# Optimization experiments

Measured on AMD Instinct MI355X. Metric: run time of the kernel, lower is better.

Reference implementation:

```python
import jax, jax.numpy as jnp
import numpy as np

TOPK = 2


def _conv2d(x, w, b):
    # x: (B, Cin, H, W), w: (Cout, Cin, 3, 3), SAME padding (padding=1)
    y = jax.lax.conv_general_dilated(
        x, w, window_strides=(1, 1), padding='SAME',
        dimension_numbers=('NCHW', 'OIHW', 'NCHW'))
    return y + b[None, :, None, None]


def _msunit(x2d, c1w, c1b, c2w, c2b):
    # TimesNet-style 2D unit: conv(1->d_model) -> GELU -> conv(d_model->1)
    h = jax.nn.gelu(_conv2d(x2d, c1w, c1b))
    return _conv2d(h, c2w, c2b)


def setup_inputs():
    B, T, H, DM = 256, 2048, 720, 64
    key = jax.random.key(0)
    ks = jax.random.split(key, 5)
    x = jax.random.normal(ks[0], (B, 1, T), jnp.float32)
    conv1_w = jax.random.normal(ks[1], (DM, 1, 3, 3), jnp.float32) * 0.1
    conv1_b = jnp.zeros((DM,), jnp.float32)
    conv2_w = jax.random.normal(ks[2], (1, DM, 3, 3), jnp.float32) * 0.1
    conv2_b = jnp.zeros((1,), jnp.float32)
    head_w = jax.random.normal(ks[3], (H, T), jnp.float32) * 0.02
    head_b = jnp.zeros((H,), jnp.float32)
    return {'x': x, 'conv1_w': conv1_w, 'conv1_b': conv1_b,
            'conv2_w': conv2_w, 'conv2_b': conv2_b,
            'head_w': head_w, 'head_b': head_b}


def reference(x, conv1_w, conv1_b, conv2_w, conv2_b, head_w, head_b):
    B, _, T = x.shape
    # FFT amplitude spectrum, batch-averaged, drop DC bin
    amp = jnp.abs(jnp.fft.rfft(x[:, 0, :], axis=-1)).mean(0)[1:]
    vals, idx = jax.lax.top_k(amp, TOPK)
    # data-dependent period selection (mirrors .item() calls in torch -> Python ints)
    freqs = np.asarray(idx) + 1
    P_list = [max(1, int(round(T / int(f)))) for f in freqs]
    weights = jax.nn.softmax(vals.astype(x.dtype))
    y = jnp.zeros_like(x)
    for i, P in enumerate(P_list):
        cols = (T + P - 1) // P
        pad = P * cols - T
        xp = jnp.pad(x, ((0, 0), (0, 0), (0, pad)))
        x2d = xp.reshape(B, 1, cols, P).transpose(0, 1, 3, 2)  # (B,1,P,cols)
        y2d = _msunit(x2d, conv1_w, conv1_b, conv2_w, conv2_b)  # (B,1,P,cols)
        y1d = y2d.transpose(0, 1, 3, 2).reshape(B, 1, cols * P)[..., :T]
        y = y + weights[i] * y1d
    out = y[:, 0, :] @ head_w.T + head_b  # (B, horizon)
    return out
```

## Files before the change

### kernel.cpp

```cpp
#include <hip/hip_runtime.h>
#include <math.h>

#define T_LEN   2048
#define NB      256
#define N_FREQ  1024
#define DMODEL  64
#define HORIZON 720

#define WS_AMP  64
#define WS_Y0   2048
#define WS_Y1   (2048 + NB * T_LEN)

#define PMAX_FAST 191
#define CHUNK   1024
#define NCHUNK  2
#define HSTRIDE 1412
#define ZSLOT   1408
#define XSMAX   1824
#define ZXS     (XSMAX - 1)

typedef _Float16 h4 __attribute__((ext_vector_type(4)));
typedef float    fx4 __attribute__((ext_vector_type(4)));

__device__ __forceinline__ float gelu_fast(float a) {
    float a2 = a * a;
    float z  = a * fmaf(-0.07135481627159498f, a2, -1.5957691216057308f);
    float e  = __expf(z);
    return a * __builtin_amdgcn_rcpf(1.0f + e);
}

__device__ __forceinline__ float2 cmul(float2 a, float2 b) {
    return make_float2(a.x * b.x - a.y * b.y, a.x * b.y + a.y * b.x);
}

__device__ __forceinline__ unsigned magic_div(unsigned d) {
    return (unsigned)((0x100000000ULL + d - 1) / d);
}

__device__ __forceinline__ void compute_meta(const float* __restrict__ amp,
                                             float* sf, int* si, int tid,
                                             int& P1, int& cols1, int& P2, int& cols2,
                                             float& wg1, float& wg2) {
    float* v1s = sf;        float* v2s = sf + 256;
    int*   i1s = si;        int*   i2s = si + 256;
    float4 v4 = ((const float4*)amp)[tid];
    float vv[4] = {v4.x, v4.y, v4.z, v4.w};
    float v1 = -1e30f, v2 = -1e30f; int i1 = 1 << 30, i2 = 1 << 30;
    #pragma unroll
    for (int u = 0; u < 4; ++u) {
        int j = tid * 4 + u;
        float v = vv[u];
        if (v > v1) { v2 = v1; i2 = i1; v1 = v; i1 = j; }
        else if (v > v2) { v2 = v; i2 = j; }
    }
    v1s[tid] = v1; i1s[tid] = i1; v2s[tid] = v2; i2s[tid] = i2;
    __syncthreads();
    for (int st = 128; st > 0; st >>= 1) {
        if (tid < st) {
            float w1 = v1s[tid + st]; int j1 = i1s[tid + st];
            float w2 = v2s[tid + st]; int j2 = i2s[tid + st];
            float a1 = v1s[tid];      int a1i = i1s[tid];
            float a2 = v2s[tid];      int a2i = i2s[tid];
            float n1, n2; int n1i, n2i;
            bool w1_first = (w1 > a1) || (w1 == a1 && j1 < a1i);
            if (w1_first) {
                n1 = w1; n1i = j1;
                bool a1_next = (a1 > w2) || (a1 == w2 && a1i < j2);
                if (a1_next) { n2 = a1; n2i = a1i; } else { n2 = w2; n2i = j2; }
            } else {
                n1 = a1; n1i = a1i;
                bool w1_next = (w1 > a2) || (w1 == a2 && j1 < a2i);
                if (w1_next) { n2 = w1; n2i = j1; } else { n2 = a2; n2i = a2i; }
            }
            v1s[tid] = n1; i1s[tid] = n1i; v2s[tid] = n2; i2s[tid] = n2i;
        }
        __syncthreads();
    }
    float v1f = v1s[0], v2f = v2s[0];
    int f1 = i1s[0] + 1, f2 = i2s[0] + 1;
    __syncthreads();
    P1 = (int)llround(2048.0 / (double)f1); if (P1 < 1) P1 = 1;
    P2 = (int)llround(2048.0 / (double)f2); if (P2 < 1) P2 = 1;
    cols1 = (T_LEN + P1 - 1) / P1;
    cols2 = (T_LEN + P2 - 1) / P2;
    float mx = fmaxf(v1f, v2f);
    float e1 = __expf(v1f - mx), e2 = __expf(v2f - mx);
    float inv = 1.0f / (e1 + e2);
    wg1 = e1 * inv; wg2 = e2 * inv;
}

__global__ __launch_bounds__(256) void fft_amp_kernel(const float* __restrict__ x,
                                                      float* __restrict__ amp,
                                                      float* __restrict__ out) {
    __shared__ float2 buf0[1024];
    __shared__ float2 buf1[1024];
    __shared__ float2 tw[512];
    const int tid = threadIdx.x;
    const int b = blockIdx.x;

    if (tid < 180) {
        const int zi = b * 180 + tid;
        ((float4*)out)[zi] = make_float4(0.f, 0.f, 0.f, 0.f);
    }

    {
        float s, c;
        __sincosf((float)tid * 6.135923151542565e-3f, &s, &c);
        tw[tid] = make_float2(c, -s);
        __sincosf((float)(tid + 256) * 6.135923151542565e-3f, &s, &c);
        tw[tid + 256] = make_float2(c, -s);
    }
    const float2* xz = (const float2*)(x + b * T_LEN);
    buf0[tid]       = xz[tid];
    buf0[tid + 256] = xz[tid + 256];
    buf0[tid + 512] = xz[tid + 512];
    buf0[tid + 768] = xz[tid + 768];
    __syncthreads();

    float2* src = buf0;
    float2* dst = buf1;
    for (int s = 0; s < 10; s += 2) {
        const int Ns = 1 << s;
        const int j1 = tid;
        const int q  = j1 & (Ns - 1);
        const int hi = j1 >> s;
        float2 A = src[j1];
        float2 B = src[j1 + 512];
        float2 C = src[j1 + 256];
        float2 D = src[j1 + 768];
        float2 w  = tw[q << (9 - s)];
        float2 wB = cmul(w, B);
        float2 wD = cmul(w, D);
        float2 P0 = make_float2(A.x + wB.x, A.y + wB.y);
        float2 P1 = make_float2(A.x - wB.x, A.y - wB.y);
        float2 Q0 = make_float2(C.x + wD.x, C.y + wD.y);
        float2 Q1 = make_float2(C.x - wD.x, C.y - wD.y);
        float2 wa = tw[q << (8 - s)];
        float2 wb = tw[(q + Ns) << (8 - s)];
        float2 t0 = cmul(wa, Q0);
        float2 t1 = cmul(wb, Q1);
        const int O = (hi << (s + 2)) + q;
        dst[O]          = make_float2(P0.x + t0.x, P0.y + t0.y);
        dst[O + 2 * Ns] = make_float2(P0.x - t0.x, P0.y - t0.y);
        dst[O + Ns]     = make_float2(P1.x + t1.x, P1.y + t1.y);
        dst[O + 3 * Ns] = make_float2(P1.x - t1.x, P1.y - t1.y);
        __syncthreads();
        float2* tmp = src; src = dst; dst = tmp;
    }
    const int rot = (b * 8) & 1023;
    #pragma unroll
    for (int j = 0; j < 4; ++j) {
        const int kk = (tid + j * 256 + rot) & 1023;
        const int k  = kk + 1;
        float mag;
        if (k == 1024) {
            float2 Z0 = src[0];
            mag = fabsf(Z0.x - Z0.y) * (1.0f / 256.0f);
        } else {
            float2 Zk = src[k];
            float2 Zn = src[1024 - k];
            float Ax = 0.5f * (Zk.x + Zn.x), Ay = 0.5f * (Zk.y - Zn.y);
            float Bx = 0.5f * (Zk.y + Zn.y), By = -0.5f * (Zk.x - Zn.x);
            float sn, cs;
            __sincosf((float)k * 3.0679615757712823e-3f, &sn, &cs);
            float Xx = Ax + cs * Bx + sn * By;
            float Xy = Ay + cs * By - sn * Bx;
            mag = sqrtf(Xx * Xx + Xy * Xy) * (1.0f / 256.0f);
        }
        atomicAdd(amp + kk, mag);
    }
}

__global__ __launch_bounds__(256) void conv_fast_kernel(
    const float* __restrict__ x,
    const float* __restrict__ w1, const float* __restrict__ b1,
    const float* __restrict__ w2, const float* __restrict__ b2,
    const float* __restrict__ amp,
    float* __restrict__ ws)
{
    __shared__ float xs[XSMAX];
    __shared__ _Float16 dk[9][HSTRIDE];

    const int tid = threadIdx.x;

    int P1, cols1, P2, cols2; float wg1, wg2;
    compute_meta(amp, xs, (int*)(xs + 512), tid, P1, cols1, P2, cols2, wg1, wg2);

    if (blockIdx.x == 0 && blockIdx.y == 0 && tid == 0) {
        int* mi = (int*)ws;
        mi[0] = P1; mi[1] = cols1; mi[2] = P2; mi[3] = cols2;
        ws[4] = wg1; ws[5] = wg2;
    }

    const int per  = blockIdx.y;
    const int P    = per == 0 ? P1 : P2;
    const int cols = per == 0 ? cols1 : cols2;
    if (P > PMAX_FAST || P < 2) return;
    const float wgt = per == 0 ? wg1 : wg2;
    float* yout = ws + (per == 0 ? WS_Y0 : WS_Y1);

    const int b   = blockIdx.x >> 1;
    const int ci  = blockIdx.x & 1;
    const int t0  = ci * CHUNK;
    const int U0  = t0 - (P + 1);
    const int HN  = CHUNK + 2 * P + 2;
    const int X0  = t0 - (2 * P + 2);
    const int XN  = CHUNK + 4 * P + 4;
    const unsigned MP = magic_div((unsigned)P);

    __syncthreads();
    const int bT = b * T_LEN;
    for (int j = tid; j < XSMAX; j += 256) {
        int t = X0 + j;
        xs[j] = (j < XN && t >= 0 && t < T_LEN) ? x[bT + t] : 0.f;
    }
    __syncthreads();

    const int lane = tid & 63;
    const int wv   = tid >> 6;
    const int lm   = lane & 15;
    const int lg   = lane >> 4;

    h4  w1f[4], w2f[4];
    fx4 b1f[4];
    #pragma unroll
    for (int t = 0; t < 4; ++t) {
        #pragma unroll
        for (int i = 0; i < 4; ++i) {
            const int k = lg * 4 + i;
            w1f[t][i] = (_Float16)((k < 9) ? w1[(t * 16 + lm) * 9 + k] : 0.f);
            w2f[t][i] = (_Float16)((lm < 9) ? w2[(t * 16 + k) * 9 + lm] : 0.f);
            b1f[t][i] = b1[t * 16 + k];
        }
    }

    const int HN16 = (HN + 15) >> 4;
    const fx4 zf4 = {0.f, 0.f, 0.f, 0.f};

    for (int nt = wv; nt < HN16; nt += 4) {
        const int ih = nt * 16 + lm;
        const int u  = U0 + ih;
        const int uu = u < 0 ? 0 : u;
        const int cc = (int)__umulhi((unsigned)uu, MP);
        const int pp = uu - cc * P;
        const bool rm = pp > 0, rp = pp < P - 1, cm = cc > 0, cp = (cc + 1) < cols;
        const int ibase = ih + P + 1;
        h4 xb;
        #pragma unroll
        for (int j = 0; j < 4; ++j) {
            const int tap = lg * 4 + j;
            const int q = (tap * 86) >> 8;
            const int r = tap - q * 3;
            const bool ok = (tap < 9)
                && (q > 0 || rm) && (q < 2 || rp)
                && (r > 0 || cm) && (r < 2 || cp);
            const int addr = ok ? (ibase + (r - 1) * P + (q - 1)) : ZXS;
            xb[j] = (_Float16)xs[addr];
        }
        fx4 h0 = __builtin_amdgcn_mfma_f32_16x16x16f16(w1f[0], xb, b1f[0], 0, 0, 0);
        fx4 h1 = __builtin_amdgcn_mfma_f32_16x16x16f16(w1f[1], xb, b1f[1], 0, 0, 0);
        fx4 h2 = __builtin_amdgcn_mfma_f32_16x16x16f16(w1f[2], xb, b1f[2], 0, 0, 0);
        fx4 h3 = __builtin_amdgcn_mfma_f32_16x16x16f16(w1f[3], xb, b1f[3], 0, 0, 0);
        h4 g0, g1, g2, g3;
        #pragma unroll
        for (int i = 0; i < 4; ++i) {
            g0[i] = (_Float16)gelu_fast(h0[i]);
            g1[i] = (_Float16)gelu_fast(h1[i]);
            g2[i] = (_Float16)gelu_fast(h2[i]);
            g3[i] = (_Float16)gelu_fast(h3[i]);
        }
        fx4 da = __builtin_amdgcn_mfma_f32_16x16x16f16(w2f[0], g0, zf4, 0, 0, 0);
        fx4 db = __builtin_amdgcn_mfma_f32_16x16x16f16(w2f[1], g1, zf4, 0, 0, 0);
        da = __builtin_amdgcn_mfma_f32_16x16x16f16(w2f[2], g2, da, 0, 0, 0);
        db = __builtin_amdgcn_mfma_f32_16x16x16f16(w2f[3], g3, db, 0, 0, 0);
        if (ih < HN) {
            #pragma unroll
            for (int i = 0; i < 4; ++i) {
                const int row = lg * 4 + i;
                if (row < 9) dk[row][ih] = (_Float16)(da[i] + db[i]);
            }
        }
    }
    if (tid < 9) dk[tid][ZSLOT] = (_Float16)0.f;
    __syncthreads();

    const float bias2 = b2[0];
    #pragma unroll
    for (int o = 0; o < 4; ++o) {
        const int t = t0 + tid + o * 256;
        const int iout = tid + o * 256 + (P + 1);
        const int cc = (int)__umulhi((unsigned)t, MP);
        const int pp = t - cc * P;
        const bool rm = pp > 0, rp = pp < P - 1, cm = cc > 0, cp = (cc + 1) < cols;
        const int i0 = (rm && cm) ? iout - P - 1 : ZSLOT;
        const int i1 = rm         ? iout - 1     : ZSLOT;
        const int i2 = (rm && cp) ? iout + P - 1 : ZSLOT;
        const int i3 = cm         ? iout - P     : ZSLOT;
        const int i5 = cp         ? iout + P     : ZSLOT;
        const int i6 = (rp && cm) ? iout - P + 1 : ZSLOT;
        const int i7 = rp         ? iout + 1     : ZSLOT;
        const int i8 = (rp && cp) ? iout + P + 1 : ZSLOT;
        float s = (float)dk[4][iout];
        s += (float)dk[0][i0]; s += (float)dk[1][i1]; s += (float)dk[2][i2];
        s += (float)dk[3][i3]; s += (float)dk[5][i5]; s += (float)dk[6][i6];
        s += (float)dk[7][i7]; s += (float)dk[8][i8];
        yout[bT + t] = wgt * (s + bias2);
    }
}

__global__ __launch_bounds__(256) void conv_unit_kernel(
    const float* __restrict__ x,
    const float* __restrict__ w1, const float* __restrict__ b1,
    const float* __restrict__ w2, const float* __restrict__ b2,
    float* __restrict__ ws)
{
    const int* mi = (const int*)ws;
    const int per   = blockIdx.y;
    const int P     = mi[per * 2 + 0];
    const int cols  = mi[per * 2 + 1];
    if (P <= PMAX_FAST && P >= 2) return;
    const float wgt = ws[4 + per];
    float* yout = ws + (per == 0 ? WS_Y0 : WS_Y1);

    __shared__ float w1s[DMODEL * 9];
    __shared__ float w2s[DMODEL * 9];
    __shared__ float b1s[DMODEL];
    __shared__ float xs[12][13];
    __shared__ float hs[DMODEL][101];

    const int tid = threadIdx.x;
    for (int i = tid; i < DMODEL * 9; i += 256) { w1s[i] = w1[i]; w2s[i] = w2[i]; }
    if (tid < DMODEL) b1s[tid] = b1[tid];
    const float bias2 = b2[0];

    const int tp = (P + 7) >> 3;
    const int tc = (cols + 7) >> 3;
    const int tiles_img = tp * tc;
    const int total = tiles_img * NB;

    for (int tile = blockIdx.x; tile < total; tile += gridDim.x) {
        const int b   = tile / tiles_img;
        const int ti  = tile - b * tiles_img;
        const int tpi = ti / tc;
        const int tci = ti - tpi * tc;
        const int p0 = tpi * 8, c0 = tci * 8;

        __syncthreads();
        if (tid < 144) {
            int i = tid / 12, j = tid - (tid / 12) * 12;
            int pp = p0 - 2 + i, cc = c0 - 2 + j;
            float v = 0.f;
            if (pp >= 0 && pp < P && cc >= 0 && cc < cols) {
                int t = cc * P + pp;
                if (t < T_LEN) v = x[b * T_LEN + t];
            }
            xs[i][j] = v;
        }
        __syncthreads();

        #pragma unroll
        for (int it = 0; it < 25; ++it) {
            int idx = it * 256 + tid;
            int ch = idx / 100;
            int px = idx - ch * 100;
            int pi = px / 10;
            int pj = px - pi * 10;
            const float* w = &w1s[ch * 9];
            float a = b1s[ch];
            a = fmaf(w[0], xs[pi    ][pj    ], a);
            a = fmaf(w[1], xs[pi    ][pj + 1], a);
            a = fmaf(w[2], xs[pi    ][pj + 2], a);
            a = fmaf(w[3], xs[pi + 1][pj    ], a);
            a = fmaf(w[4], xs[pi + 1][pj + 1], a);
            a = fmaf(w[5], xs[pi + 1][pj + 2], a);
            a = fmaf(w[6], xs[pi + 2][pj    ], a);
            a = fmaf(w[7], xs[pi + 2][pj + 1], a);
            a = fmaf(w[8], xs[pi + 2][pj + 2], a);
            float g = gelu_fast(a);
            int pp = p0 - 1 + pi, cc = c0 - 1 + pj;
            bool in_img = (pp >= 0) & (pp < P) & (cc >= 0) & (cc < cols);
            hs[ch][px] = in_img ? g : 0.0f;
        }
        __syncthreads();

        {
            const int pixel = tid >> 2, part = tid & 3;
            const int pi = pixel >> 3, pj = pixel & 7;
            const int base = pi * 10 + pj;
            float s = 0.f;
            for (int ch = part * 16; ch < part * 16 + 16; ++ch) {
                const float* w  = &w2s[ch * 9];
                const float* hr = &hs[ch][base];
                s = fmaf(w[0], hr[0],  s);
                s = fmaf(w[1], hr[1],  s);
                s = fmaf(w[2], hr[2],  s);
                s = fmaf(w[3], hr[10], s);
                s = fmaf(w[4], hr[11], s);
                s = fmaf(w[5], hr[12], s);
                s = fmaf(w[6], hr[20], s);
                s = fmaf(w[7], hr[21], s);
                s = fmaf(w[8], hr[22], s);
            }
            s += __shfl_down(s, 1);
            s += __shfl_down(s, 2);
            if (part == 0) {
                int pp = p0 + pi, cc = c0 + pj;
                if (pp < P && cc < cols) {
                    int t = cc * P + pp;
                    if (t < T_LEN) yout[b * T_LEN + t] = wgt * (s + bias2);
                }
            }
        }
    }
}

#define HG_KC 256
__global__ __launch_bounds__(256) void head_gemm_kernel(
    const float* __restrict__ ws, const float* __restrict__ hw,
    const float* __restrict__ hb, float* __restrict__ out)
{
    __shared__ _Float16 As[32][72];
    __shared__ _Float16 Bs[32][72];
    const float* y0 = ws + WS_Y0;
    const float* y1 = ws + WS_Y1;
    const int tid = threadIdx.x;
    const int b0 = blockIdx.x * 32, h0 = blockIdx.y * 32;
    const int kc0 = blockIdx.z * HG_KC;
    const int lane = tid & 63;
    const int wv   = tid >> 6;
    const int lm   = lane & 15;
    const int lg   = lane >> 4;
    const int wm   = (wv & 1) * 16;
    const int wn   = (wv >> 1) * 16;
    const int sr = tid >> 4;
    const int sq = (tid & 15) * 4;

    fx4 acc = {0.f, 0.f, 0.f, 0.f};

    for (int k0 = kc0; k0 < kc0 + HG_KC; k0 += 64) {
        #pragma unroll
        for (int hh = 0; hh < 2; ++hh) {
            const int r = sr + hh * 16;
            const int src = (b0 + r) * T_LEN + k0 + sq;
            float4 u = *(const float4*)(y0 + src);
            float4 v = *(const float4*)(y1 + src);
            As[r][sq + 0] = (_Float16)(u.x + v.x);
            As[r][sq + 1] = (_Float16)(u.y + v.y);
            As[r][sq + 2] = (_Float16)(u.z + v.z);
            As[r][sq + 3] = (_Float16)(u.w + v.w);
            const int hr = h0 + r;
            float4 w = (hr < HORIZON) ? *(const float4*)(hw + hr * T_LEN + k0 + sq)
                                      : make_float4(0.f, 0.f, 0.f, 0.f);
            Bs[r][sq + 0] = (_Float16)w.x;
            Bs[r][sq + 1] = (_Float16)w.y;
            Bs[r][sq + 2] = (_Float16)w.z;
            Bs[r][sq + 3] = (_Float16)w.w;
        }
        __syncthreads();
        #pragma unroll
        for (int kk = 0; kk < 64; kk += 16) {
            h4 af = *(const h4*)&As[wm + lm][kk + lg * 4];
            h4 bf = *(const h4*)&Bs[wn + lm][kk + lg * 4];
            acc = __builtin_amdgcn_mfma_f32_16x16x16f16(af, bf, acc, 0, 0, 0);
        }
        __syncthreads();
    }
    const int ncol = h0 + wn + lm;
    if (ncol < HORIZON) {
        const float bb = (blockIdx.z == 0) ? hb[ncol] : 0.f;
        #pragma unroll
        for (int i = 0; i < 4; ++i) {
            const int m = b0 + wm + lg * 4 + i;
            atomicAdd(&out[m * HORIZON + ncol], acc[i] + bb);
        }
    }
}

extern "C" void kernel_launch(void* const* d_in, const int* in_sizes, int n_in,
                              void* d_out, int out_size, void* d_ws, size_t ws_size,
                              hipStream_t stream) {
    const float* x   = (const float*)d_in[0];
    const float* c1w = (const float*)d_in[1];
    const float* c1b = (const float*)d_in[2];
    const float* c2w = (const float*)d_in[3];
    const float* c2b = (const float*)d_in[4];
    const float* hw  = (const float*)d_in[5];
    const float* hb  = (const float*)d_in[6];
    float* out = (float*)d_out;
    float* ws  = (float*)d_ws;

    float* amp = ws + WS_AMP;

    hipMemsetAsync(amp, 0, N_FREQ * sizeof(float), stream);
    fft_amp_kernel<<<NB, 256, 0, stream>>>(x, amp, out);
    conv_fast_kernel<<<dim3(NB * NCHUNK, 2), 256, 0, stream>>>(x, c1w, c1b, c2w, c2b, amp, ws);
    conv_unit_kernel<<<dim3(256, 2), 256, 0, stream>>>(x, c1w, c1b, c2w, c2b, ws);
    head_gemm_kernel<<<dim3(NB / 32, (HORIZON + 31) / 32, T_LEN / HG_KC), 256, 0, stream>>>(ws, hw, hb, out);
}
```

Before: 136.7 us.

## Compute GELU in packed half2 and stage input window as fp16

```diff
diff --git a/kernel.cpp b/kernel.cpp
--- a/kernel.cpp
+++ b/kernel.cpp
@@ -1,4 +1,5 @@
 #include <hip/hip_runtime.h>
+#include <hip/hip_fp16.h>
 #include <math.h>
 
 #define T_LEN   2048
@@ -16,8 +17,8 @@
 #define NCHUNK  2
 #define HSTRIDE 1412
 #define ZSLOT   1408
-#define XSMAX   1824
-#define ZXS     (XSMAX - 1)
+#define XS2N    1796
+#define ZXS     1795
 
 typedef _Float16 h4 __attribute__((ext_vector_type(4)));
 typedef float    fx4 __attribute__((ext_vector_type(4)));
@@ -27,6 +28,24 @@
     float z  = a * fmaf(-0.07135481627159498f, a2, -1.5957691216057308f);
     float e  = __expf(z);
     return a * __builtin_amdgcn_rcpf(1.0f + e);
+}
+
+__device__ __forceinline__ __half2 gelu2(float x, float y) {
+    __half2 a  = __float22half2_rn(make_float2(x, y));
+    __half2 a2 = __hmul2(a, a);
+    const __half2 c2 = __float2half2_rn(-0.07135481627159498f);
+    const __half2 c1 = __float2half2_rn(-1.5957691216057308f);
+    __half2 z = __hmul2(a, __hfma2(c2, a2, c1));
+    __half2 e = h2exp(z);
+    const __half2 one = __float2half2_rn(1.0f);
+    return __hmul2(a, h2rcp(__hadd2(one, e)));
+}
+
+__device__ __forceinline__ h4 gelu4(fx4 h) {
+    union { __half2 p[2]; h4 v; } u;
+    u.p[0] = gelu2(h[0], h[1]);
+    u.p[1] = gelu2(h[2], h[3]);
+    return u.v;
 }
 
 __device__ __forceinline__ float2 cmul(float2 a, float2 b) {
@@ -178,13 +197,22 @@
     const float* __restrict__ amp,
     float* __restrict__ ws)
 {
-    __shared__ float xs[XSMAX];
-    __shared__ _Float16 dk[9][HSTRIDE];
+    __shared__ __align__(16) _Float16 xs2[XS2N];
+    __shared__ __align__(16) _Float16 dk[9][HSTRIDE];
 
     const int tid = threadIdx.x;
+    const int b   = blockIdx.x >> 1;
+    const int ci  = blockIdx.x & 1;
+    const int t0  = ci * CHUNK;
+    const int bT  = b * T_LEN;
+
+    for (int j = tid; j < XS2N; j += 256) {
+        const int t = t0 - 384 + j;
+        xs2[j] = (_Float16)((j < 1792 && t >= 0 && t < T_LEN) ? x[bT + t] : 0.f);
+    }
 
     int P1, cols1, P2, cols2; float wg1, wg2;
-    compute_meta(amp, xs, (int*)(xs + 512), tid, P1, cols1, P2, cols2, wg1, wg2);
+    compute_meta(amp, (float*)dk, (int*)dk + 512, tid, P1, cols1, P2, cols2, wg1, wg2);
 
     if (blockIdx.x == 0 && blockIdx.y == 0 && tid == 0) {
         int* mi = (int*)ws;
@@ -199,22 +227,10 @@
     const float wgt = per == 0 ? wg1 : wg2;
     float* yout = ws + (per == 0 ? WS_Y0 : WS_Y1);
 
-    const int b   = blockIdx.x >> 1;
-    const int ci  = blockIdx.x & 1;
-    const int t0  = ci * CHUNK;
     const int U0  = t0 - (P + 1);
     const int HN  = CHUNK + 2 * P + 2;
-    const int X0  = t0 - (2 * P + 2);
-    const int XN  = CHUNK + 4 * P + 4;
     const unsigned MP = magic_div((unsigned)P);
-
-    __syncthreads();
-    const int bT = b * T_LEN;
-    for (int j = tid; j < XSMAX; j += 256) {
-        int t = X0 + j;
-        xs[j] = (j < XN && t >= 0 && t < T_LEN) ? x[bT + t] : 0.f;
-    }
-    __syncthreads();
+    const int IB0 = 383 - P;
 
     const int lane = tid & 63;
     const int wv   = tid >> 6;
@@ -244,7 +260,7 @@
         const int cc = (int)__umulhi((unsigned)uu, MP);
         const int pp = uu - cc * P;
         const bool rm = pp > 0, rp = pp < P - 1, cm = cc > 0, cp = (cc + 1) < cols;
-        const int ibase = ih + P + 1;
+        const int ibase = ih + IB0;
         h4 xb;
         #pragma unroll
         for (int j = 0; j < 4; ++j) {
@@ -255,20 +271,16 @@
                 && (q > 0 || rm) && (q < 2 || rp)
                 && (r > 0 || cm) && (r < 2 || cp);
             const int addr = ok ? (ibase + (r - 1) * P + (q - 1)) : ZXS;
-            xb[j] = (_Float16)xs[addr];
+            xb[j] = xs2[addr];
         }
         fx4 h0 = __builtin_amdgcn_mfma_f32_16x16x16f16(w1f[0], xb, b1f[0], 0, 0, 0);
         fx4 h1 = __builtin_amdgcn_mfma_f32_16x16x16f16(w1f[1], xb, b1f[1], 0, 0, 0);
         fx4 h2 = __builtin_amdgcn_mfma_f32_16x16x16f16(w1f[2], xb, b1f[2], 0, 0, 0);
         fx4 h3 = __builtin_amdgcn_mfma_f32_16x16x16f16(w1f[3], xb, b1f[3], 0, 0, 0);
-        h4 g0, g1, g2, g3;
-        #pragma unroll
-        for (int i = 0; i < 4; ++i) {
-            g0[i] = (_Float16)gelu_fast(h0[i]);
-            g1[i] = (_Float16)gelu_fast(h1[i]);
-            g2[i] = (_Float16)gelu_fast(h2[i]);
-            g3[i] = (_Float16)gelu_fast(h3[i]);
-        }
+        h4 g0 = gelu4(h0);
+        h4 g1 = gelu4(h1);
+        h4 g2 = gelu4(h2);
+        h4 g3 = gelu4(h3);
         fx4 da = __builtin_amdgcn_mfma_f32_16x16x16f16(w2f[0], g0, zf4, 0, 0, 0);
         fx4 db = __builtin_amdgcn_mfma_f32_16x16x16f16(w2f[1], g1, zf4, 0, 0, 0);
         da = __builtin_amdgcn_mfma_f32_16x16x16f16(w2f[2], g2, da, 0, 0, 0);
```

Measured after the change: 135.9 us. Within noise of the previous version (-0.6%).
